# Performance work log

Hardware: AMD Instinct MI355X
Metric: run time of the kernel (lower is better)

## Reference

```python
import jax, jax.numpy as jnp
import numpy as np

B, S, D_IN, D_OUT = 2, 4096, 512, 512


def setup_inputs() -> dict:
    key = jax.random.key(0)
    k1, k2, k3, k4 = jax.random.split(key, 4)
    x = jax.random.normal(k1, (B, S, D_IN), dtype=jnp.float32)
    # weights stored as [d_in, d_out] so projection is x @ W
    W_query = jax.random.normal(k2, (D_IN, D_OUT), dtype=jnp.float32) * (D_IN ** -0.5)
    W_key = jax.random.normal(k3, (D_IN, D_OUT), dtype=jnp.float32) * (D_IN ** -0.5)
    W_value = jax.random.normal(k4, (D_IN, D_OUT), dtype=jnp.float32) * (D_IN ** -0.5)
    return {"x": x, "W_query": W_query, "W_key": W_key, "W_value": W_value}


def reference(x, W_query, W_key, W_value):
    # Faithful to source: masked_fill is called non-in-place and its result
    # discarded, so NO causal mask is actually applied. Dropout prob = 0.0.
    d_out = W_query.shape[-1]
    q = jnp.einsum('bsi,io->bso', x, W_query)  # [B,S,D_OUT]
    k = jnp.einsum('bsi,io->bso', x, W_key)
    v = jnp.einsum('bsi,io->bso', x, W_value)
    scores = jnp.einsum('bqd,bkd->bqk', q, k) / jnp.sqrt(jnp.float32(d_out))
    weights = jax.nn.softmax(scores, axis=-1)  # [B,S,S]
    context = jnp.einsum('bqk,bkd->bqd', weights, v)  # [B,S,D_OUT]
    return context
```

## Files before the change

### kernel.cpp

```cpp
#include <hip/hip_runtime.h>
#include <cstdint>
#include <cstddef>

typedef unsigned short u16;
typedef __attribute__((ext_vector_type(8))) short bf16x8;
typedef __attribute__((ext_vector_type(4))) float f32x4;

struct alignas(8) u16x4_t { u16 x, y, z, w; };

__device__ __forceinline__ u16 f2bf(float f) {
  uint32_t u = __builtin_bit_cast(uint32_t, f);
  u += 0x7FFFu + ((u >> 16) & 1u);
  return (u16)(u >> 16);
}
__device__ __forceinline__ float bf2f(u16 h) {
  uint32_t u = ((uint32_t)h) << 16;
  return __builtin_bit_cast(float, u);
}

__device__ __forceinline__ void g2l16(const u16* g, u16* l) {
  __builtin_amdgcn_global_load_lds(
      (const __attribute__((address_space(1))) void*)g,
      (__attribute__((address_space(3))) void*)l, 16, 0, 0);
}

#define S_WAITCNT_VM(N) \
  __builtin_amdgcn_s_waitcnt((((N) & 0xF)) | (0x7 << 4) | (0xF << 8) | ((((N) >> 4) & 3) << 14))
#define S_WAITCNT_LGKM0 __builtin_amdgcn_s_waitcnt(0xC07F)

template <int DEPTH, int BM, int BN>
__device__ __forceinline__ void gemm_bt_pipe(
    const u16* __restrict__ A, const u16* __restrict__ Bt,
    int lda, int ldb, int kIters, int m0, int n0,
    u16* sh, f32x4 (&acc)[BM / 32][BN / 32]) {
  constexpr int MI = BM / 32;
  constexpr int NI = BN / 32;
  constexpr int T = (BM + BN) / 64;
  constexpr int SLOT = (BM + BN) * 32;
  constexpr int WVM = T * (DEPTH - 1);
  const int tid = threadIdx.x;
  const int lane = tid & 63, wave = tid >> 6;
  const int wm = wave >> 1, wn = wave & 1, lr = lane & 15, quad = lane >> 4;

  const u16* gp[T];
#pragma unroll
  for (int t = 0; t < T; ++t) {
    const int c = t * 256 + wave * 64 + lane;
    if (c < BM * 4) {
      const int r = c >> 2;
      const int s = (c & 3) ^ ((r >> 1) & 3);
      gp[t] = A + (size_t)(m0 + r) * lda + s * 8;
    } else {
      const int cb = c - BM * 4;
      const int r = cb >> 2;
      const int s = (cb & 3) ^ ((r >> 1) & 3);
      gp[t] = Bt + (size_t)(n0 + r) * ldb + s * 8;
    }
  }
  const int wo = wave * 512;

  auto issue = [&](int slot, int kb) {
    u16* s = sh + slot * SLOT;
#pragma unroll
    for (int t = 0; t < T; ++t)
      g2l16(gp[t] + kb, s + t * 2048 + wo);
  };

#pragma unroll
  for (int p = 0; p < DEPTH; ++p)
    issue(p, (p < kIters ? p : kIters - 1) * 32);

  const int xq = (quad ^ ((lr >> 1) & 3)) * 8;
  for (int kt = 0; kt < kIters; ++kt) {
    S_WAITCNT_VM(WVM);
    __builtin_amdgcn_s_barrier();
    u16* slot = sh + (kt % DEPTH) * SLOT;
    u16* sB = slot + BM * 32;
    bf16x8 af[MI], bfr[NI];
#pragma unroll
    for (int mi = 0; mi < MI; ++mi)
      af[mi] = *(const bf16x8*)(slot + ((wm * (BM / 2) + mi * 16 + lr) * 32 + xq));
#pragma unroll
    for (int ni = 0; ni < NI; ++ni)
      bfr[ni] = *(const bf16x8*)(sB + ((wn * (BN / 2) + ni * 16 + lr) * 32 + xq));
    S_WAITCNT_LGKM0;
    __builtin_amdgcn_s_barrier();
    const int kn = kt + DEPTH;
    issue(kn % DEPTH, (kn < kIters ? kn : kIters - 1) * 32);
#pragma unroll
    for (int mi = 0; mi < MI; ++mi)
#pragma unroll
      for (int ni = 0; ni < NI; ++ni)
        acc[mi][ni] = __builtin_amdgcn_mfma_f32_16x16x32_bf16(af[mi], bfr[ni], acc[mi][ni], 0, 0, 0);
  }
}

#define ZERO_ACC4(acc)                        \
  _Pragma("unroll") for (int mi = 0; mi < 4; ++mi) \
  _Pragma("unroll") for (int ni = 0; ni < 4; ++ni) \
      acc[mi][ni] = f32x4{0.f, 0.f, 0.f, 0.f};

__device__ __forceinline__ void epilogue_ct16(
    const f32x4 (&acc)[4][4], u16* __restrict__ base, int m0w, int n0w,
    int ld, int lane, bool do_exp, float scale, float* rs) {
  const int lr = lane & 15, quad = lane >> 4;
  const int j = quad >> 1, par = quad & 1;
#pragma unroll
  for (int mp = 0; mp < 2; ++mp) {
#pragma unroll
    for (int ni = 0; ni < 4; ++ni) {
      uint32_t p0[2], p1[2];
#pragma unroll
      for (int h = 0; h < 2; ++h) {
        const f32x4 v = acc[mp * 2 + h][ni];
        float e0, e1, e2, e3;
        if (do_exp) {
          e0 = __expf(v[0] * scale); e1 = __expf(v[1] * scale);
          e2 = __expf(v[2] * scale); e3 = __expf(v[3] * scale);
        } else {
          e0 = v[0]; e1 = v[1]; e2 = v[2]; e3 = v[3];
        }
        const u16 h0 = f2bf(e0), h1 = f2bf(e1), h2 = f2bf(e2), h3 = f2bf(e3);
        p0[h] = (uint32_t)h0 | ((uint32_t)h1 << 16);
        p1[h] = (uint32_t)h2 | ((uint32_t)h3 << 16);
        if (rs) rs[ni] += bf2f(h0) + bf2f(h1) + bf2f(h2) + bf2f(h3);
      }
      const uint32_t s0 = par ? p0[0] : p0[1];
      const uint32_t s1 = par ? p1[0] : p1[1];
      const uint32_t r0 = (uint32_t)__shfl_xor((int)s0, 16);
      const uint32_t r1 = (uint32_t)__shfl_xor((int)s1, 16);
      uint4 st;
      if (!par) { st.x = p0[0]; st.y = p1[0]; st.z = r0;    st.w = r1;    }
      else      { st.x = r0;    st.y = r1;    st.z = p0[1]; st.w = p1[1]; }
      const int m = m0w + 16 * (mp * 2 + par) + 8 * j;
      const int n = n0w + ni * 16 + lr;
      *(uint4*)(base + (size_t)n * ld + m) = st;
    }
  }
}

__global__ __launch_bounds__(256) void convert_x(const float* __restrict__ x,
                                                 u16* __restrict__ Xb) {
  const int i = (blockIdx.x * 256 + threadIdx.x) * 4;
  const float4 v = *(const float4*)(x + i);
  u16x4_t h;
  h.x = f2bf(v.x); h.y = f2bf(v.y); h.z = f2bf(v.z); h.w = f2bf(v.w);
  *(u16x4_t*)(Xb + i) = h;
}

__global__ __launch_bounds__(256) void transpose_w(const float* __restrict__ W0,
                                                   const float* __restrict__ W1,
                                                   const float* __restrict__ W2,
                                                   u16* __restrict__ Wt) {
  __shared__ float tile[32][33];
  const float* W = blockIdx.z == 0 ? W0 : (blockIdx.z == 1 ? W1 : W2);
  u16* out = Wt + (size_t)blockIdx.z * 512 * 512;
  const int bx = blockIdx.x * 32;
  const int by = blockIdx.y * 32;
  const int tx = threadIdx.x, ty = threadIdx.y;
#pragma unroll
  for (int i = 0; i < 32; i += 8)
    tile[ty + i][tx] = W[(size_t)(by + ty + i) * 512 + bx + tx];
  __syncthreads();
#pragma unroll
  for (int i = 0; i < 32; i += 8)
    out[(size_t)(bx + ty + i) * 512 + by + tx] = f2bf(tile[tx][ty + i]);
}

__global__ __launch_bounds__(256) void qkv_kernel(
    const u16* __restrict__ Xb, const u16* __restrict__ Wt,
    u16* __restrict__ Qb, u16* __restrict__ Kb, u16* __restrict__ Vt) {
  __shared__ u16 sh[2 * 8192];
  const int z = blockIdx.z;
  int m0, n0;
  const u16 *A, *Bt;
  if (z < 2) {
    m0 = blockIdx.y * 128;
    n0 = blockIdx.x * 128;
    A = Wt + (size_t)z * 512 * 512;
    Bt = Xb;
  } else {
    m0 = blockIdx.x * 128;
    n0 = blockIdx.y * 128;
    A = Xb;
    Bt = Wt + (size_t)2 * 512 * 512;
  }
  f32x4 acc[4][4];
  ZERO_ACC4(acc);
  gemm_bt_pipe<2, 128, 128>(A, Bt, 512, 512, 16, m0, n0, sh, acc);

  const int lane = threadIdx.x & 63, wave = threadIdx.x >> 6;
  const int wm = wave >> 1, wn = wave & 1;
  if (z < 2) {
    epilogue_ct16(acc, z == 0 ? Qb : Kb, m0 + wm * 64, n0 + wn * 64, 512,
                  lane, false, 1.f, nullptr);
  } else {
    const int bb = m0 >> 12;
    epilogue_ct16(acc, Vt + (size_t)bb * 512 * 4096,
                  (m0 & 4095) + wm * 64, n0 + wn * 64, 4096,
                  lane, false, 1.f, nullptr);
  }
}

__global__ __launch_bounds__(256) void scores_kernel(
    const u16* __restrict__ Qb, const u16* __restrict__ Kb,
    u16* __restrict__ P, float* __restrict__ L) {
  __shared__ u16 sh[2 * 8192];
  const int b = blockIdx.z;
  const int m0 = blockIdx.y * 128;
  const int n0 = blockIdx.x * 128;
  f32x4 acc[4][4];
  ZERO_ACC4(acc);
  gemm_bt_pipe<2, 128, 128>(Kb + (size_t)b * 4096 * 512, Qb + (size_t)b * 4096 * 512,
                            512, 512, 16, m0, n0, sh, acc);

  const int lane = threadIdx.x & 63, wave = threadIdx.x >> 6;
  const int wm = wave >> 1, wn = wave & 1, lr = lane & 15, quad = lane >> 4;
  const float scale = 0.04419417382415922f;
  u16* Pb = P + (size_t)b * 4096 * 4096;

  float rs[4] = {0.f, 0.f, 0.f, 0.f};
  epilogue_ct16(acc, Pb, m0 + wm * 64, n0 + wn * 64, 4096, lane, true, scale, rs);

#pragma unroll
  for (int ni = 0; ni < 4; ++ni) {
    float v = rs[ni];
    v += __shfl_xor(v, 16);
    v += __shfl_xor(v, 32);
    if (quad == 0)
      atomicAdd(&L[b * 4096 + n0 + wn * 64 + ni * 16 + lr], v);
  }
}

__global__ __launch_bounds__(256) void pv_kernel(
    const u16* __restrict__ P, const u16* __restrict__ Vt,
    const float* __restrict__ L, float* __restrict__ out) {
  __shared__ u16 sh[4 * 6144];
  const int b = blockIdx.z;
  const int id = blockIdx.x;
  const int ntile = (id >> 3) & 3;
  const int mtile = (id & 7) | ((id >> 5) << 3);
  const int m0 = mtile * 64;
  const int n0 = ntile * 128;
  f32x4 acc[2][4];
#pragma unroll
  for (int mi = 0; mi < 2; ++mi)
#pragma unroll
    for (int ni = 0; ni < 4; ++ni) acc[mi][ni] = f32x4{0.f, 0.f, 0.f, 0.f};
  gemm_bt_pipe<4, 64, 128>(P + (size_t)b * 4096 * 4096, Vt + (size_t)b * 512 * 4096,
                           4096, 4096, 128, m0, n0, sh, acc);

  const int lane = threadIdx.x & 63, wave = threadIdx.x >> 6;
  const int wm = wave >> 1, wn = wave & 1, lr = lane & 15, quad = lane >> 4;
#pragma unroll
  for (int mi = 0; mi < 2; ++mi) {
    const int row = m0 + wm * 32 + mi * 16 + quad * 4;
    float rinv[4];
#pragma unroll
    for (int i = 0; i < 4; ++i) rinv[i] = 1.0f / L[b * 4096 + row + i];
#pragma unroll
    for (int ni = 0; ni < 4; ++ni) {
      const int col = n0 + wn * 64 + ni * 16 + lr;
#pragma unroll
      for (int i = 0; i < 4; ++i)
        out[(size_t)b * 2097152 + (size_t)(row + i) * 512 + col] =
            acc[mi][ni][i] * rinv[i];
    }
  }
}

extern "C" void kernel_launch(void* const* d_in, const int* in_sizes, int n_in,
                              void* d_out, int out_size, void* d_ws, size_t ws_size,
                              hipStream_t stream) {
  const float* x  = (const float*)d_in[0];
  const float* Wq = (const float*)d_in[1];
  const float* Wk = (const float*)d_in[2];
  const float* Wv = (const float*)d_in[3];
  float* out = (float*)d_out;
  char* ws = (char*)d_ws;
  u16* Xb = (u16*)(ws);
  u16* Qb = (u16*)(ws + 8388608);
  u16* Kb = (u16*)(ws + 16777216);
  u16* Vt = (u16*)(ws + 25165824);
  u16* Wt = (u16*)(ws + 33554432);
  u16* P  = (u16*)(ws + 35127296);
  float* L = (float*)(ws + 102236160);

  convert_x<<<4096, 256, 0, stream>>>(x, Xb);
  transpose_w<<<dim3(16, 16, 3), dim3(32, 8), 0, stream>>>(Wq, Wk, Wv, Wt);
  qkv_kernel<<<dim3(64, 4, 3), 256, 0, stream>>>(Xb, Wt, Qb, Kb, Vt);
  hipMemsetAsync(L, 0, 8192 * sizeof(float), stream);
  scores_kernel<<<dim3(32, 32, 2), 256, 0, stream>>>(Qb, Kb, P, L);
  pv_kernel<<<dim3(256, 1, 2), 256, 0, stream>>>(P, Vt, L, out);
}
```

Baseline: 200.0 us.

## Split PV GEMM over K with reduce pass and merge prep kernels

The PV GEMM is split into two K halves, doubling the grid to 1024 blocks so more CUs stay busy. Each half writes an unnormalized partial: one into a reused workspace buffer (the old Q/K region), the other into the output. A new reduce kernel sums the two partials and applies the softmax row normalization. The x-conversion and weight-transpose kernels are also merged into one launch, saving a launch. The cost is extra fp32 partial traffic, one more kernel, and a pipeline depth cut from 4 to 3 stages.

```diff
diff --git a/kernel.cpp b/kernel.cpp
--- a/kernel.cpp
+++ b/kernel.cpp
@@ -139,25 +139,27 @@
   }
 }
 
-__global__ __launch_bounds__(256) void convert_x(const float* __restrict__ x,
-                                                 u16* __restrict__ Xb) {
-  const int i = (blockIdx.x * 256 + threadIdx.x) * 4;
-  const float4 v = *(const float4*)(x + i);
-  u16x4_t h;
-  h.x = f2bf(v.x); h.y = f2bf(v.y); h.z = f2bf(v.z); h.w = f2bf(v.w);
-  *(u16x4_t*)(Xb + i) = h;
-}
-
-__global__ __launch_bounds__(256) void transpose_w(const float* __restrict__ W0,
-                                                   const float* __restrict__ W1,
-                                                   const float* __restrict__ W2,
-                                                   u16* __restrict__ Wt) {
+__global__ __launch_bounds__(256) void prep_kernel(
+    const float* __restrict__ x, u16* __restrict__ Xb,
+    const float* __restrict__ W0, const float* __restrict__ W1,
+    const float* __restrict__ W2, u16* __restrict__ Wt) {
   __shared__ float tile[32][33];
-  const float* W = blockIdx.z == 0 ? W0 : (blockIdx.z == 1 ? W1 : W2);
-  u16* out = Wt + (size_t)blockIdx.z * 512 * 512;
-  const int bx = blockIdx.x * 32;
-  const int by = blockIdx.y * 32;
-  const int tx = threadIdx.x, ty = threadIdx.y;
+  const int id = blockIdx.x;
+  if (id < 4096) {
+    const int i = (id * 256 + threadIdx.x) * 4;
+    const float4 v = *(const float4*)(x + i);
+    u16x4_t h;
+    h.x = f2bf(v.x); h.y = f2bf(v.y); h.z = f2bf(v.z); h.w = f2bf(v.w);
+    *(u16x4_t*)(Xb + i) = h;
+    return;
+  }
+  const int t = id - 4096;
+  const int wz = t >> 8, rem = t & 255;
+  const float* W = wz == 0 ? W0 : (wz == 1 ? W1 : W2);
+  u16* out = Wt + (size_t)wz * 512 * 512;
+  const int bx = (rem & 15) * 32;
+  const int by = (rem >> 4) * 32;
+  const int tx = threadIdx.x & 31, ty = threadIdx.x >> 5;
 #pragma unroll
   for (int i = 0; i < 32; i += 8)
     tile[ty + i][tx] = W[(size_t)(by + ty + i) * 512 + bx + tx];
@@ -234,39 +236,52 @@
 
 __global__ __launch_bounds__(256) void pv_kernel(
     const u16* __restrict__ P, const u16* __restrict__ Vt,
-    const float* __restrict__ L, float* __restrict__ out) {
-  __shared__ u16 sh[4 * 6144];
+    float* __restrict__ part0, float* __restrict__ out) {
+  __shared__ u16 sh[3 * 6144];
   const int b = blockIdx.z;
   const int id = blockIdx.x;
   const int ntile = (id >> 3) & 3;
-  const int mtile = (id & 7) | ((id >> 5) << 3);
+  const int ks = (id >> 5) & 1;
+  const int mtile = (id & 7) | ((id >> 6) << 3);
   const int m0 = mtile * 64;
   const int n0 = ntile * 128;
+  const int k0 = ks * 2048;
   f32x4 acc[2][4];
 #pragma unroll
   for (int mi = 0; mi < 2; ++mi)
 #pragma unroll
     for (int ni = 0; ni < 4; ++ni) acc[mi][ni] = f32x4{0.f, 0.f, 0.f, 0.f};
-  gemm_bt_pipe<4, 64, 128>(P + (size_t)b * 4096 * 4096, Vt + (size_t)b * 512 * 4096,
-                           4096, 4096, 128, m0, n0, sh, acc);
+  gemm_bt_pipe<3, 64, 128>(P + (size_t)b * 4096 * 4096 + k0,
+                           Vt + (size_t)b * 512 * 4096 + k0,
+                           4096, 4096, 64, m0, n0, sh, acc);
 
   const int lane = threadIdx.x & 63, wave = threadIdx.x >> 6;
   const int wm = wave >> 1, wn = wave & 1, lr = lane & 15, quad = lane >> 4;
+  float* dst = ks ? out : part0;
 #pragma unroll
   for (int mi = 0; mi < 2; ++mi) {
     const int row = m0 + wm * 32 + mi * 16 + quad * 4;
-    float rinv[4];
-#pragma unroll
-    for (int i = 0; i < 4; ++i) rinv[i] = 1.0f / L[b * 4096 + row + i];
 #pragma unroll
     for (int ni = 0; ni < 4; ++ni) {
       const int col = n0 + wn * 64 + ni * 16 + lr;
 #pragma unroll
       for (int i = 0; i < 4; ++i)
-        out[(size_t)b * 2097152 + (size_t)(row + i) * 512 + col] =
-            acc[mi][ni][i] * rinv[i];
+        dst[(size_t)b * 2097152 + (size_t)(row + i) * 512 + col] = acc[mi][ni][i];
     }
   }
+}
+
+__global__ __launch_bounds__(256) void reduce_kernel(
+    const float* __restrict__ part0, const float* __restrict__ L,
+    float* __restrict__ out) {
+  const int i = (blockIdx.x * 256 + threadIdx.x) * 4;
+  const float rinv = 1.0f / L[i >> 9];
+  const float4 a = *(const float4*)(out + i);
+  const float4 p = *(const float4*)(part0 + i);
+  float4 r;
+  r.x = (a.x + p.x) * rinv; r.y = (a.y + p.y) * rinv;
+  r.z = (a.z + p.z) * rinv; r.w = (a.w + p.w) * rinv;
+  *(float4*)(out + i) = r;
 }
 
 extern "C" void kernel_launch(void* const* d_in, const int* in_sizes, int n_in,
@@ -285,11 +300,12 @@
   u16* Wt = (u16*)(ws + 33554432);
   u16* P  = (u16*)(ws + 35127296);
   float* L = (float*)(ws + 102236160);
-
-  convert_x<<<4096, 256, 0, stream>>>(x, Xb);
-  transpose_w<<<dim3(16, 16, 3), dim3(32, 8), 0, stream>>>(Wq, Wk, Wv, Wt);
+  float* part0 = (float*)(ws + 8388608);
+
+  prep_kernel<<<4864, 256, 0, stream>>>(x, Xb, Wq, Wk, Wv, Wt);
   qkv_kernel<<<dim3(64, 4, 3), 256, 0, stream>>>(Xb, Wt, Qb, Kb, Vt);
   hipMemsetAsync(L, 0, 8192 * sizeof(float), stream);
   scores_kernel<<<dim3(32, 32, 2), 256, 0, stream>>>(Qb, Kb, P, L);
-  pv_kernel<<<dim3(256, 1, 2), 256, 0, stream>>>(P, Vt, L, out);
-}
+  pv_kernel<<<dim3(512, 1, 2), 256, 0, stream>>>(P, Vt, part0, out);
+  reduce_kernel<<<4096, 256, 0, stream>>>(part0, L, out);
+}
```

Measured after the change: 211.9 us. +6.0%, slower.
